# Kernel tuning notes

Hardware: AMD Instinct MI355X
Metric: run time of the kernel (lower is better)

The kernel has to match this reference:

```python
import jax, jax.numpy as jnp
import numpy as np

N_NODES = 100000
N_EDGES = 1600000
D_IN = 128
D_OUT = 128
EPS = 1e-5


def setup_inputs() -> dict:
    key = jax.random.key(0)
    ks = jax.random.split(key, 5)
    x = jax.random.normal(ks[0], (N_NODES, D_IN), dtype=jnp.float32)
    edge_index = jax.random.randint(ks[1], (2, N_EDGES), 0, N_NODES, dtype=jnp.int64)
    scale = 1.0 / np.sqrt(D_IN)
    W_root = jax.random.normal(ks[2], (D_IN, D_OUT), dtype=jnp.float32) * scale
    W_rel = jax.random.normal(ks[3], (D_IN, D_OUT), dtype=jnp.float32) * scale
    b_rel = jax.random.normal(ks[4], (D_OUT,), dtype=jnp.float32) * 0.01
    gamma = jnp.ones((D_OUT,), dtype=jnp.float32)
    beta = jnp.zeros((D_OUT,), dtype=jnp.float32)
    return {"x": x, "edge_index": edge_index, "W_root": W_root, "W_rel": W_rel,
            "b_rel": b_rel, "gamma": gamma, "beta": beta}


def reference(x, edge_index, W_root, W_rel, b_rel, gamma, beta):
    # GraphConv: out = aggr(x_j) @ W_rel + b_rel + x @ W_root   (aggr = sum)
    src = edge_index[0]
    dst = edge_index[1]
    aggr = jax.ops.segment_sum(x[src], dst, num_segments=x.shape[0])  # [N, D_IN]
    h = aggr @ W_rel + b_rel + x @ W_root                              # [N, D_OUT]
    # NodeLevelBatchNorm (training mode: batch stats over node dim, biased var)
    mean = jnp.mean(h, axis=0)
    var = jnp.mean(jnp.square(h - mean), axis=0)
    h_norm = (h - mean) * jax.lax.rsqrt(var + EPS) * gamma + beta
    return jax.nn.relu(h_norm)
```

## Files before the change

kernel.cpp:

```cpp
#include <hip/hip_runtime.h>

#define N_NODES 100000
#define N_EDGES 1600000
#define D 128
#define NB 196
#define EPT 10
#define CHUNK 2560
#define BIN_BLOCKS 625
#define CVT_X_BLOCKS 6250
#define ZROW N_NODES
#define PBK 13312

typedef __bf16 bf16x8 __attribute__((ext_vector_type(8)));
typedef float f32x4 __attribute__((ext_vector_type(4)));

__device__ __forceinline__ unsigned f2bf(float f) {
    unsigned u = __float_as_uint(f);
    return (u + 0x7fffu + ((u >> 16) & 1u)) >> 16;
}
__device__ __forceinline__ float bf_lo(unsigned u) { return __uint_as_float(u << 16); }
__device__ __forceinline__ float bf_hi(unsigned u) { return __uint_as_float(u & 0xffff0000u); }

__global__ __launch_bounds__(256) void prep_kernel(const float* __restrict__ x,
                                                   const float* __restrict__ Wrel,
                                                   const float* __restrict__ Wroot,
                                                   unsigned short* __restrict__ x_bf,
                                                   unsigned short* __restrict__ Wt,
                                                   int* __restrict__ bcur) {
    int b = blockIdx.x;
    int t = threadIdx.x;
    if (b < CVT_X_BLOCKS) {
        size_t i = ((size_t)b * 256 + t) * 8;
        float4 v0 = *(const float4*)(x + i);
        float4 v1 = *(const float4*)(x + i + 4);
        uint4 p;
        p.x = f2bf(v0.x) | (f2bf(v0.y) << 16);
        p.y = f2bf(v0.z) | (f2bf(v0.w) << 16);
        p.z = f2bf(v1.x) | (f2bf(v1.y) << 16);
        p.w = f2bf(v1.z) | (f2bf(v1.w) << 16);
        *(uint4*)(x_bf + i) = p;
    } else if (b < CVT_X_BLOCKS + 128) {
        int c = b - CVT_X_BLOCKS;
        float v = (t < 128) ? Wrel[t * D + c] : Wroot[(t - 128) * D + c];
        Wt[c * 256 + t] = (unsigned short)f2bf(v);
    } else if (b == CVT_X_BLOCKS + 128) {
        if (t < 16) *(uint4*)(x_bf + (size_t)ZROW * D + t * 8) = make_uint4(0, 0, 0, 0);
    } else {
        bcur[t] = t * PBK;
    }
}

__global__ __launch_bounds__(256) void binify_kernel(const int* __restrict__ ei,
                                                     int* __restrict__ bcur,
                                                     unsigned* __restrict__ epk) {
    __shared__ int lhist[256];
    __shared__ int lstart[256];
    __shared__ int lfill[256];
    __shared__ int gbase[256];
    __shared__ uint2 stage[CHUNK];

    int t = threadIdx.x;
    int base = blockIdx.x * CHUNK;
    lhist[t] = 0;
    lfill[t] = 0;
    __syncthreads();

    int src[EPT], dst[EPT];
#pragma unroll
    for (int i = 0; i < EPT; ++i) {
        int e = base + i * 256 + t;
        src[i] = ei[e];
        dst[i] = ei[N_EDGES + e];
        atomicAdd(&lhist[dst[i] >> 9], 1);
    }
    __syncthreads();

    int v = lhist[t];
    lstart[t] = v;
    __syncthreads();
    for (int off = 1; off < 256; off <<= 1) {
        int a = (t >= off) ? lstart[t - off] : 0;
        __syncthreads();
        lstart[t] += a;
        __syncthreads();
    }
    int excl = lstart[t] - v;
    if (t < NB && v > 0) gbase[t] = atomicAdd(&bcur[t], v);
    __syncthreads();
    lstart[t] = excl;
    __syncthreads();

#pragma unroll
    for (int i = 0; i < EPT; ++i) {
        int b = dst[i] >> 9;
        int lp = atomicAdd(&lfill[b], 1);
        stage[lstart[b] + lp] = make_uint2((unsigned)src[i], (unsigned)dst[i]);
    }
    __syncthreads();

    for (int i = t; i < CHUNK; i += 256) {
        uint2 p = stage[i];
        int b = (int)(p.y >> 9);
        unsigned code = p.x | ((p.y & 511u) << 17);
        epk[gbase[b] + (i - lstart[b])] = code;
    }
}

__global__ __launch_bounds__(512) void place_kernel(const unsigned* __restrict__ epk,
                                                    const int* __restrict__ bcur,
                                                    int* __restrict__ rbeg,
                                                    int* __restrict__ rend,
                                                    int* __restrict__ srcs) {
    __shared__ int cnt[512];
    __shared__ int s[512];
    __shared__ int cursor[512];
    int b = blockIdx.x;
    int t = threadIdx.x;
    int R = b * PBK;
    int pbeg = R;
    int pend = bcur[b];

    cnt[t] = 0;
    __syncthreads();
    for (int i = pbeg + t; i < pend; i += 512)
        atomicAdd(&cnt[epk[i] >> 17], 1);
    __syncthreads();

    int v = (cnt[t] + 7) & ~7;
    s[t] = v;
    __syncthreads();
    for (int off = 1; off < 512; off <<= 1) {
        int a = (t >= off) ? s[t - off] : 0;
        __syncthreads();
        s[t] += a;
        __syncthreads();
    }
    int st = R + s[t] - v;
    int g = (b << 9) + t;
    if (g < 100352) { rbeg[g] = st; rend[g] = st + v; }
    cursor[t] = st;
    __syncthreads();

    for (int i = pbeg + t; i < pend; i += 512) {
        unsigned code = epk[i];
        int pos = atomicAdd(&cursor[code >> 17], 1);
        srcs[pos] = (int)(code & 0x1FFFFu);
    }
    __syncthreads();

    int endp = st + v;
    for (int p = cursor[t]; p < endp; ++p) srcs[p] = ZROW;
}

__global__ __launch_bounds__(256) void fused_gemm(const unsigned short* __restrict__ x_bf,
                                                  const int* __restrict__ rbeg,
                                                  const int* __restrict__ rend,
                                                  const int* __restrict__ srcs,
                                                  const unsigned short* __restrict__ Wt,
                                                  const float* __restrict__ brel,
                                                  unsigned short* __restrict__ h_bf,
                                                  float* __restrict__ gsum,
                                                  float* __restrict__ gss) {
    __shared__ unsigned short Af[2048 * 8];
    __shared__ unsigned short Bf[2048 * 8];
    __shared__ float sbias[128];
    __shared__ float SredS[4][128];
    __shared__ float SredQ[4][128];

    const int t = threadIdx.x;
    const int wave = t >> 6;
    const int lane = t & 63;
    const int quad = lane >> 4;
    const int l16 = lane & 15;
    const int blockRow = blockIdx.x * 128;

    if (t < 128) sbias[t] = brel[t];

#pragma unroll
    for (int f = t; f < 2048; f += 256) {
        int kcl = f >> 9;
        int ct = (f >> 6) & 7;
        int ln = f & 63;
        int col = ct * 16 + (ln & 15);
        int kb = kcl * 32 + ((ln >> 4) << 3);
        *(uint4*)&Bf[f * 8] = *(const uint4*)(Wt + col * 256 + kb);
    }

    const unsigned short* xp = x_bf + l16 * 8;
#pragma unroll 1
    for (int g = 0; g < 8; ++g) {
        int r = wave * 32 + g * 4 + quad;
        int node = blockRow + r;
        int e = rbeg[node];
        int end = rend[node];
        float a0 = 0.f, a1 = 0.f, a2 = 0.f, a3 = 0.f;
        float a4 = 0.f, a5 = 0.f, a6 = 0.f, a7 = 0.f;
        for (; e < end; e += 8) {
            int4 s0 = *(const int4*)(srcs + e);
            int4 s1 = *(const int4*)(srcs + e + 4);
            uint4 u0 = *(const uint4*)(xp + (size_t)s0.x * D);
            uint4 u1 = *(const uint4*)(xp + (size_t)s0.y * D);
            uint4 u2 = *(const uint4*)(xp + (size_t)s0.z * D);
            uint4 u3 = *(const uint4*)(xp + (size_t)s0.w * D);
            uint4 u4 = *(const uint4*)(xp + (size_t)s1.x * D);
            uint4 u5 = *(const uint4*)(xp + (size_t)s1.y * D);
            uint4 u6 = *(const uint4*)(xp + (size_t)s1.z * D);
            uint4 u7 = *(const uint4*)(xp + (size_t)s1.w * D);
            a0 += bf_lo(u0.x) + bf_lo(u1.x) + bf_lo(u2.x) + bf_lo(u3.x)
                + bf_lo(u4.x) + bf_lo(u5.x) + bf_lo(u6.x) + bf_lo(u7.x);
            a1 += bf_hi(u0.x) + bf_hi(u1.x) + bf_hi(u2.x) + bf_hi(u3.x)
                + bf_hi(u4.x) + bf_hi(u5.x) + bf_hi(u6.x) + bf_hi(u7.x);
            a2 += bf_lo(u0.y) + bf_lo(u1.y) + bf_lo(u2.y) + bf_lo(u3.y)
                + bf_lo(u4.y) + bf_lo(u5.y) + bf_lo(u6.y) + bf_lo(u7.y);
            a3 += bf_hi(u0.y) + bf_hi(u1.y) + bf_hi(u2.y) + bf_hi(u3.y)
                + bf_hi(u4.y) + bf_hi(u5.y) + bf_hi(u6.y) + bf_hi(u7.y);
            a4 += bf_lo(u0.z) + bf_lo(u1.z) + bf_lo(u2.z) + bf_lo(u3.z)
                + bf_lo(u4.z) + bf_lo(u5.z) + bf_lo(u6.z) + bf_lo(u7.z);
            a5 += bf_hi(u0.z) + bf_hi(u1.z) + bf_hi(u2.z) + bf_hi(u3.z)
                + bf_hi(u4.z) + bf_hi(u5.z) + bf_hi(u6.z) + bf_hi(u7.z);
            a6 += bf_lo(u0.w) + bf_lo(u1.w) + bf_lo(u2.w) + bf_lo(u3.w)
                + bf_lo(u4.w) + bf_lo(u5.w) + bf_lo(u6.w) + bf_lo(u7.w);
            a7 += bf_hi(u0.w) + bf_hi(u1.w) + bf_hi(u2.w) + bf_hi(u3.w)
                + bf_hi(u4.w) + bf_hi(u5.w) + bf_hi(u6.w) + bf_hi(u7.w);
        }
        uint4 w;
        w.x = f2bf(a0) | (f2bf(a1) << 16);
        w.y = f2bf(a2) | (f2bf(a3) << 16);
        w.z = f2bf(a4) | (f2bf(a5) << 16);
        w.w = f2bf(a6) | (f2bf(a7) << 16);
        int c = l16;
        int wf = ((r >> 5) << 3) + (((r >> 4) & 1) << 2) + (c >> 2);
        int L = ((c & 3) << 4) | ((r & 15) ^ (c & 3));
        *(uint4*)&Af[(wf * 64 + L) * 8] = w;
    }
    __syncthreads();

    f32x4 acc[2][8];
#pragma unroll
    for (int i = 0; i < 2; ++i)
#pragma unroll
        for (int j = 0; j < 8; ++j) acc[i][j] = (f32x4){0.f, 0.f, 0.f, 0.f};

    const int Lr = (quad << 4) | (l16 ^ quad);

#pragma unroll
    for (int kcl = 0; kcl < 4; ++kcl) {
        bf16x8 af0 = *(const bf16x8*)&Af[(((wave << 3) + kcl) * 64 + Lr) * 8];
        bf16x8 af1 = *(const bf16x8*)&Af[(((wave << 3) + 4 + kcl) * 64 + Lr) * 8];
#pragma unroll
        for (int ct = 0; ct < 8; ++ct) {
            bf16x8 bfrag = *(const bf16x8*)&Bf[((kcl * 8 + ct) * 64 + lane) * 8];
            acc[0][ct] = __builtin_amdgcn_mfma_f32_16x16x32_bf16(af0, bfrag, acc[0][ct], 0, 0, 0);
            acc[1][ct] = __builtin_amdgcn_mfma_f32_16x16x32_bf16(af1, bfrag, acc[1][ct], 0, 0, 0);
        }
    }
    __syncthreads();

#pragma unroll
    for (int f = t; f < 2048; f += 256) {
        int kcl = f >> 9;
        int ct = (f >> 6) & 7;
        int ln = f & 63;
        int col = ct * 16 + (ln & 15);
        int kb = 128 + kcl * 32 + ((ln >> 4) << 3);
        *(uint4*)&Bf[f * 8] = *(const uint4*)(Wt + col * 256 + kb);
    }
    __syncthreads();

    const int rowb = blockRow + wave * 32;
#pragma unroll
    for (int kcl = 0; kcl < 4; ++kcl) {
        const int k0 = kcl * 32 + quad * 8;
        bf16x8 af0 = *(const bf16x8*)(x_bf + (size_t)(rowb + l16) * D + k0);
        bf16x8 af1 = *(const bf16x8*)(x_bf + (size_t)(rowb + 16 + l16) * D + k0);
#pragma unroll
        for (int ct = 0; ct < 8; ++ct) {
            bf16x8 bfrag = *(const bf16x8*)&Bf[((kcl * 8 + ct) * 64 + lane) * 8];
            acc[0][ct] = __builtin_amdgcn_mfma_f32_16x16x32_bf16(af0, bfrag, acc[0][ct], 0, 0, 0);
            acc[1][ct] = __builtin_amdgcn_mfma_f32_16x16x32_bf16(af1, bfrag, acc[1][ct], 0, 0, 0);
        }
    }

    float csum[8], css[8];
#pragma unroll
    for (int ct = 0; ct < 8; ++ct) { csum[ct] = 0.f; css[ct] = 0.f; }

#pragma unroll
    for (int rt = 0; rt < 2; ++rt) {
#pragma unroll
        for (int ct = 0; ct < 8; ++ct) {
            int col = ct * 16 + l16;
            float bv = sbias[col];
#pragma unroll
            for (int reg = 0; reg < 4; ++reg) {
                int row = blockRow + wave * 32 + rt * 16 + quad * 4 + reg;
                if (row < N_NODES) {
                    float v = acc[rt][ct][reg] + bv;
                    h_bf[(size_t)row * D + col] = (unsigned short)f2bf(v);
                    csum[ct] += v;
                    css[ct] += v * v;
                }
            }
        }
    }
#pragma unroll
    for (int ct = 0; ct < 8; ++ct) {
        float s = csum[ct], q = css[ct];
        s += __shfl_xor(s, 16);
        s += __shfl_xor(s, 32);
        q += __shfl_xor(q, 16);
        q += __shfl_xor(q, 32);
        if (quad == 0) {
            SredS[wave][ct * 16 + l16] = s;
            SredQ[wave][ct * 16 + l16] = q;
        }
    }
    __syncthreads();
    if (t < 128) {
        float s = SredS[0][t] + SredS[1][t] + SredS[2][t] + SredS[3][t];
        float q = SredQ[0][t] + SredQ[1][t] + SredQ[2][t] + SredQ[3][t];
        unsafeAtomicAdd(&gsum[t], s);
        unsafeAtomicAdd(&gss[t], q);
    }
}

__global__ __launch_bounds__(256) void norm_kernel(const unsigned short* __restrict__ h_bf,
                                                   float* __restrict__ out,
                                                   const float* __restrict__ gsum,
                                                   const float* __restrict__ gss,
                                                   const float* __restrict__ gamma,
                                                   const float* __restrict__ beta) {
    __shared__ float sscale[128];
    __shared__ float sshift[128];
    int t = threadIdx.x;
    if (t < 128) {
        const float inv_n = 1.0f / (float)N_NODES;
        float mean = gsum[t] * inv_n;
        float var = gss[t] * inv_n - mean * mean;
        float rs = rsqrtf(var + 1e-5f);
        float sc = gamma[t] * rs;
        sscale[t] = sc;
        sshift[t] = beta[t] - mean * sc;
    }
    __syncthreads();
    size_t e = ((size_t)blockIdx.x * 256 + t) * 4;
    if (e >= (size_t)N_NODES * D) return;
    int c = (int)(e & 127);
    uint2 u = *(const uint2*)(h_bf + e);
    float4 v;
    v.x = fmaxf(bf_lo(u.x) * sscale[c + 0] + sshift[c + 0], 0.f);
    v.y = fmaxf(bf_hi(u.x) * sscale[c + 1] + sshift[c + 1], 0.f);
    v.z = fmaxf(bf_lo(u.y) * sscale[c + 2] + sshift[c + 2], 0.f);
    v.w = fmaxf(bf_hi(u.y) * sscale[c + 3] + sshift[c + 3], 0.f);
    *(float4*)(out + e) = v;
}

extern "C" void kernel_launch(void* const* d_in, const int* in_sizes, int n_in,
                              void* d_out, int out_size, void* d_ws, size_t ws_size,
                              hipStream_t stream) {
    const float* x     = (const float*)d_in[0];
    const int*   ei    = (const int*)d_in[1];
    const float* Wroot = (const float*)d_in[2];
    const float* Wrel  = (const float*)d_in[3];
    const float* brel  = (const float*)d_in[4];
    const float* gamma = (const float*)d_in[5];
    const float* beta  = (const float*)d_in[6];
    float* out = (float*)d_out;

    unsigned short* h_bf = (unsigned short*)d_ws;
    unsigned* epk = (unsigned*)d_ws;
    unsigned short* x_bf = h_bf + (size_t)N_NODES * D;
    unsigned short* Wt   = x_bf + (size_t)(N_NODES + 1) * D;
    float* gsum  = (float*)(Wt + 128 * 256);
    float* gss   = gsum + 128;
    int* bcur    = (int*)(gss + 128);
    int* rbeg    = bcur + 256;
    int* rend    = rbeg + 100352;
    int* srcs    = rend + 100352;

    hipMemsetAsync(gsum, 0, 256 * sizeof(float), stream);

    prep_kernel<<<CVT_X_BLOCKS + 130, 256, 0, stream>>>(x, Wrel, Wroot, x_bf, Wt, bcur);
    binify_kernel<<<BIN_BLOCKS, 256, 0, stream>>>(ei, bcur, epk);
    place_kernel<<<NB, 512, 0, stream>>>(epk, bcur, rbeg, rend, srcs);
    fused_gemm<<<(N_NODES + 127) / 128, 256, 0, stream>>>(
        x_bf, rbeg, rend, srcs, Wt, brel, h_bf, gsum, gss);
    norm_kernel<<<12500, 256, 0, stream>>>(h_bf, out, gsum, gss, gamma, beta);
}
```

Before: 254.9 us.

## Replace binned two-pass CSR build with global-atomic degree count and scatter

```diff
diff --git a/kernel.cpp b/kernel.cpp
--- a/kernel.cpp
+++ b/kernel.cpp
@@ -24,9 +24,10 @@
 __global__ __launch_bounds__(256) void prep_kernel(const float* __restrict__ x,
                                                    const float* __restrict__ Wrel,
                                                    const float* __restrict__ Wroot,
+                                                   const int* __restrict__ ei,
                                                    unsigned short* __restrict__ x_bf,
                                                    unsigned short* __restrict__ Wt,
-                                                   int* __restrict__ bcur) {
+                                                   int* __restrict__ deg) {
     int b = blockIdx.x;
     int t = threadIdx.x;
     if (b < CVT_X_BLOCKS) {
@@ -46,88 +47,28 @@
     } else if (b == CVT_X_BLOCKS + 128) {
         if (t < 16) *(uint4*)(x_bf + (size_t)ZROW * D + t * 8) = make_uint4(0, 0, 0, 0);
     } else {
-        bcur[t] = t * PBK;
-    }
-}
-
-__global__ __launch_bounds__(256) void binify_kernel(const int* __restrict__ ei,
-                                                     int* __restrict__ bcur,
-                                                     unsigned* __restrict__ epk) {
-    __shared__ int lhist[256];
-    __shared__ int lstart[256];
-    __shared__ int lfill[256];
-    __shared__ int gbase[256];
-    __shared__ uint2 stage[CHUNK];
-
-    int t = threadIdx.x;
-    int base = blockIdx.x * CHUNK;
-    lhist[t] = 0;
-    lfill[t] = 0;
-    __syncthreads();
-
-    int src[EPT], dst[EPT];
-#pragma unroll
-    for (int i = 0; i < EPT; ++i) {
-        int e = base + i * 256 + t;
-        src[i] = ei[e];
-        dst[i] = ei[N_EDGES + e];
-        atomicAdd(&lhist[dst[i] >> 9], 1);
-    }
-    __syncthreads();
-
-    int v = lhist[t];
-    lstart[t] = v;
-    __syncthreads();
-    for (int off = 1; off < 256; off <<= 1) {
-        int a = (t >= off) ? lstart[t - off] : 0;
-        __syncthreads();
-        lstart[t] += a;
-        __syncthreads();
-    }
-    int excl = lstart[t] - v;
-    if (t < NB && v > 0) gbase[t] = atomicAdd(&bcur[t], v);
-    __syncthreads();
-    lstart[t] = excl;
-    __syncthreads();
-
-#pragma unroll
-    for (int i = 0; i < EPT; ++i) {
-        int b = dst[i] >> 9;
-        int lp = atomicAdd(&lfill[b], 1);
-        stage[lstart[b] + lp] = make_uint2((unsigned)src[i], (unsigned)dst[i]);
-    }
-    __syncthreads();
-
-    for (int i = t; i < CHUNK; i += 256) {
-        uint2 p = stage[i];
-        int b = (int)(p.y >> 9);
-        unsigned code = p.x | ((p.y & 511u) << 17);
-        epk[gbase[b] + (i - lstart[b])] = code;
-    }
-}
-
-__global__ __launch_bounds__(512) void place_kernel(const unsigned* __restrict__ epk,
-                                                    const int* __restrict__ bcur,
-                                                    int* __restrict__ rbeg,
-                                                    int* __restrict__ rend,
-                                                    int* __restrict__ srcs) {
-    __shared__ int cnt[512];
+        int blk = b - (CVT_X_BLOCKS + 129);
+        int base = blk * CHUNK;
+#pragma unroll
+        for (int i = 0; i < EPT; ++i) {
+            int dst = ei[N_EDGES + base + i * 256 + t];
+            atomicAdd(&deg[dst], 1);
+        }
+    }
+}
+
+__global__ __launch_bounds__(512) void rowstart_kernel(const int* __restrict__ deg,
+                                                       int* __restrict__ rbeg,
+                                                       int* __restrict__ rend,
+                                                       int* __restrict__ rcur,
+                                                       int* __restrict__ srcs) {
     __shared__ int s[512];
-    __shared__ int cursor[512];
     int b = blockIdx.x;
     int t = threadIdx.x;
-    int R = b * PBK;
-    int pbeg = R;
-    int pend = bcur[b];
-
-    cnt[t] = 0;
-    __syncthreads();
-    for (int i = pbeg + t; i < pend; i += 512)
-        atomicAdd(&cnt[epk[i] >> 17], 1);
-    __syncthreads();
-
-    int v = (cnt[t] + 7) & ~7;
-    s[t] = v;
+    int g = (b << 9) + t;
+    int d = (g < N_NODES) ? deg[g] : 0;
+    int pd = (d + 7) & ~7;
+    s[t] = pd;
     __syncthreads();
     for (int off = 1; off < 512; off <<= 1) {
         int a = (t >= off) ? s[t - off] : 0;
@@ -135,21 +76,24 @@
         s[t] += a;
         __syncthreads();
     }
-    int st = R + s[t] - v;
-    int g = (b << 9) + t;
-    if (g < 100352) { rbeg[g] = st; rend[g] = st + v; }
-    cursor[t] = st;
-    __syncthreads();
-
-    for (int i = pbeg + t; i < pend; i += 512) {
-        unsigned code = epk[i];
-        int pos = atomicAdd(&cursor[code >> 17], 1);
-        srcs[pos] = (int)(code & 0x1FFFFu);
-    }
-    __syncthreads();
-
-    int endp = st + v;
-    for (int p = cursor[t]; p < endp; ++p) srcs[p] = ZROW;
+    int st = b * PBK + s[t] - pd;
+    if (g < 100352) { rbeg[g] = st; rend[g] = st + pd; rcur[g] = st; }
+    for (int p = st + d; p < st + pd; ++p) srcs[p] = ZROW;
+}
+
+__global__ __launch_bounds__(256) void scatter_kernel(const int* __restrict__ ei,
+                                                      int* __restrict__ rcur,
+                                                      int* __restrict__ srcs) {
+    int t = threadIdx.x;
+    int base = blockIdx.x * CHUNK;
+#pragma unroll
+    for (int i = 0; i < EPT; ++i) {
+        int e = base + i * 256 + t;
+        int src = ei[e];
+        int dst = ei[N_EDGES + e];
+        int pos = atomicAdd(&rcur[dst], 1);
+        srcs[pos] = src;
+    }
 }
 
 __global__ __launch_bounds__(256) void fused_gemm(const unsigned short* __restrict__ x_bf,
@@ -368,21 +312,22 @@
     float* out = (float*)d_out;
 
     unsigned short* h_bf = (unsigned short*)d_ws;
-    unsigned* epk = (unsigned*)d_ws;
     unsigned short* x_bf = h_bf + (size_t)N_NODES * D;
     unsigned short* Wt   = x_bf + (size_t)(N_NODES + 1) * D;
     float* gsum  = (float*)(Wt + 128 * 256);
     float* gss   = gsum + 128;
-    int* bcur    = (int*)(gss + 128);
-    int* rbeg    = bcur + 256;
+    int* deg     = (int*)(gss + 128);
+    int* rbeg    = deg + 100352;
     int* rend    = rbeg + 100352;
-    int* srcs    = rend + 100352;
-
-    hipMemsetAsync(gsum, 0, 256 * sizeof(float), stream);
-
-    prep_kernel<<<CVT_X_BLOCKS + 130, 256, 0, stream>>>(x, Wrel, Wroot, x_bf, Wt, bcur);
-    binify_kernel<<<BIN_BLOCKS, 256, 0, stream>>>(ei, bcur, epk);
-    place_kernel<<<NB, 512, 0, stream>>>(epk, bcur, rbeg, rend, srcs);
+    int* rcur    = rend + 100352;
+    int* srcs    = rcur + 100352;
+
+    hipMemsetAsync(gsum, 0, (256 + 100352) * sizeof(int), stream);
+
+    prep_kernel<<<CVT_X_BLOCKS + 129 + BIN_BLOCKS, 256, 0, stream>>>(
+        x, Wrel, Wroot, ei, x_bf, Wt, deg);
+    rowstart_kernel<<<NB, 512, 0, stream>>>(deg, rbeg, rend, rcur, srcs);
+    scatter_kernel<<<BIN_BLOCKS, 256, 0, stream>>>(ei, rcur, srcs);
     fused_gemm<<<(N_NODES + 127) / 128, 256, 0, stream>>>(
         x_bf, rbeg, rend, srcs, Wt, brel, h_bf, gsum, gss);
     norm_kernel<<<12500, 256, 0, stream>>>(h_bf, out, gsum, gss, gamma, beta);
```

Result: slower. 395.4 us (+55.1%).
